# Performance work log

Hardware: AMD Instinct MI355X
Metric: run time of the kernel (lower is better)

## Reference

```python
import jax, jax.numpy as jnp
import numpy as np

N_NODES = 100000
N_EDGES = 1600000
N_GRAPHS = 1024
NODE_F = 100
HID = 64
GLOB_F = 3


def setup_inputs() -> dict:
    key = jax.random.key(0)
    ks = jax.random.split(key, 16)
    s = 0.05
    return {
        "x": jax.random.normal(ks[0], (N_NODES, NODE_F), dtype=jnp.float32),
        "edge_index": jax.random.randint(ks[1], (2, N_EDGES), 0, N_NODES, dtype=jnp.int32),
        "batch": jnp.sort(jax.random.randint(ks[2], (N_NODES,), 0, N_GRAPHS, dtype=jnp.int32)),
        "global_features": jax.random.normal(ks[3], (N_GRAPHS, GLOB_F), dtype=jnp.float32),
        "W1": jax.random.normal(ks[4], (NODE_F, HID), dtype=jnp.float32) * s,
        "b1": jnp.zeros((HID,), dtype=jnp.float32),
        "W2": jax.random.normal(ks[5], (HID, HID), dtype=jnp.float32) * s,
        "b2": jnp.zeros((HID,), dtype=jnp.float32),
        "gW1": jax.random.normal(ks[6], (GLOB_F, HID), dtype=jnp.float32) * s,
        "gb1": jnp.zeros((HID,), dtype=jnp.float32),
        "gW2": jax.random.normal(ks[7], (HID, HID), dtype=jnp.float32) * s,
        "gb2": jnp.zeros((HID,), dtype=jnp.float32),
        "cW1": jax.random.normal(ks[8], (2 * HID, HID), dtype=jnp.float32) * s,
        "cb1": jnp.zeros((HID,), dtype=jnp.float32),
        "cW2": jax.random.normal(ks[9], (HID, 1), dtype=jnp.float32) * s,
        "cb2": jnp.zeros((1,), dtype=jnp.float32),
    }


def gcn_conv(x, src, dst, W, b):
    # PyG GCNConv: add self-loops, symmetric degree normalization, linear transform.
    n = x.shape[0]
    loop = jnp.arange(n, dtype=src.dtype)
    src_sl = jnp.concatenate([src, loop])
    dst_sl = jnp.concatenate([dst, loop])
    deg = jax.ops.segment_sum(jnp.ones_like(dst_sl, dtype=x.dtype), dst_sl, num_segments=n)
    dinv = deg ** -0.5  # deg >= 1 due to self-loops
    norm = dinv[src_sl] * dinv[dst_sl]  # [E+N]
    h = x @ W  # [N, HID]
    msg = h[src_sl] * norm[:, None]
    out = jax.ops.segment_sum(msg, dst_sl, num_segments=n)
    return out + b


def reference(x, edge_index, batch, global_features,
              W1, b1, W2, b2, gW1, gb1, gW2, gb2, cW1, cb1, cW2, cb2):
    src, dst = edge_index[0], edge_index[1]
    h = jax.nn.relu(gcn_conv(x, src, dst, W1, b1))
    # dropout p=0.2 is identity in eval mode
    h = gcn_conv(h, src, dst, W2, b2)
    # global mean pool over graph ids
    sums = jax.ops.segment_sum(h, batch, num_segments=N_GRAPHS)
    cnts = jax.ops.segment_sum(jnp.ones((h.shape[0],), h.dtype), batch, num_segments=N_GRAPHS)
    pooled = sums / jnp.maximum(cnts, 1.0)[:, None]  # [G, HID]
    g = jax.nn.relu(global_features @ gW1 + gb1) @ gW2 + gb2  # [G, HID]
    combined = jnp.concatenate([pooled, g], axis=1)  # [G, 2*HID]
    out = jax.nn.relu(combined @ cW1 + cb1) @ cW2 + cb2  # [G, 1]
    return out
```

## Files before the change

### kernel.cpp

```cpp
#include <hip/hip_runtime.h>

#define N_NODES  100000
#define N_EDGES  1600000
#define N_GRAPHS 1024
#define NODE_F   100
#define HID      64
#define GLOB_F   3

#define CAP      64

#define P_PART     8
#define W_PART     1024
#define R_PART     ((N_NODES + P_PART - 1) / P_PART)
#define CHUNK_PART ((N_EDGES + W_PART - 1) / W_PART)

typedef _Float16 half_t;
typedef __attribute__((ext_vector_type(8))) _Float16 half8;

__global__ void k_bucket(const int* __restrict__ src, const int* __restrict__ dst,
                         int* __restrict__ cnt, int* __restrict__ csrc_pad, int E) {
    int p = blockIdx.x % P_PART;
    int w = blockIdx.x / P_PART;
    int lo_node = p * R_PART;
    int start = w * CHUNK_PART;
    int end = start + CHUNK_PART; if (end > E) end = E;
    for (int i = start + (int)threadIdx.x; i < end; i += 256) {
        int d = dst[i];
        if ((unsigned)(d - lo_node) < (unsigned)R_PART) {
            int pos = atomicAdd(&cnt[d], 1);
            if (pos < CAP) csrc_pad[((size_t)d << 6) + pos] = src[i];
        }
    }
}

template <int K>
__launch_bounds__(256, 3)
__global__ void k_mm(const float* __restrict__ X, const float* __restrict__ W,
                     const int* __restrict__ cnt, half_t* __restrict__ Y, int N) {
    __shared__ float Xs[16 * K];
    __shared__ float dsh[16];
    int tid = threadIdx.x;
    int row0 = blockIdx.x * 16;

    const float4* Xg = reinterpret_cast<const float4*>(X + (size_t)row0 * K);
    float4* Xls = reinterpret_cast<float4*>(Xs);
    for (int i = tid; i < 16 * K / 4; i += 256) Xls[i] = Xg[i];
    if (tid < 16) dsh[tid] = 1.0f / sqrtf((float)(1 + cnt[row0 + tid]));

    int lane = tid & 63;
    int wv = tid >> 6;

    float Wr[K];
#pragma unroll
    for (int k = 0; k < K; ++k) Wr[k] = W[k * HID + lane];
    __syncthreads();

#pragma unroll
    for (int rr = 0; rr < 4; ++rr) {
        int r = row0 + wv * 4 + rr;
        const float4* xrow = reinterpret_cast<const float4*>(&Xs[(wv * 4 + rr) * K]);
        float acc0 = 0.f, acc1 = 0.f, acc2 = 0.f, acc3 = 0.f;
#pragma unroll
        for (int k4 = 0; k4 < K / 4; ++k4) {
            float4 xv = xrow[k4];
            acc0 += xv.x * Wr[k4 * 4 + 0];
            acc1 += xv.y * Wr[k4 * 4 + 1];
            acc2 += xv.z * Wr[k4 * 4 + 2];
            acc3 += xv.w * Wr[k4 * 4 + 3];
        }
        float acc = (acc0 + acc1) + (acc2 + acc3);
        Y[(size_t)r * HID + lane] = (half_t)(acc * dsh[wv * 4 + rr]);
    }
}

template <int RELU>
__global__ void k_gather(const half_t* __restrict__ Hs, const int* __restrict__ cnt,
                         const int* __restrict__ csrc_pad,
                         const float* __restrict__ b, float* __restrict__ outbuf, int N) {
    int tid = threadIdx.x;
    int d = blockIdx.x * 4 + (tid >> 6);
    if (d >= N) return;
    int lane = tid & 63;
    int g = lane >> 3;
    int l = lane & 7;
    int deg = cnt[d];
    int n = deg < CAP ? deg : CAP;
    const int* row = csrc_pad + ((size_t)d << 6);

    float acc[8] = {0, 0, 0, 0, 0, 0, 0, 0};

    int e = 0;
    for (; e + 16 <= n; e += 16) {
        int s0 = row[e + g];
        int s1 = row[e + 8 + g];
        half8 h0 = *reinterpret_cast<const half8*>(Hs + (size_t)s0 * HID + l * 8);
        half8 h1 = *reinterpret_cast<const half8*>(Hs + (size_t)s1 * HID + l * 8);
#pragma unroll
        for (int j = 0; j < 8; ++j) acc[j] += (float)h0[j];
#pragma unroll
        for (int j = 0; j < 8; ++j) acc[j] += (float)h1[j];
    }
    for (; e < n; e += 8) {
        int ee = e + g;
        if (ee < n) {
            int s = row[ee];
            half8 hv = *reinterpret_cast<const half8*>(Hs + (size_t)s * HID + l * 8);
#pragma unroll
            for (int j = 0; j < 8; ++j) acc[j] += (float)hv[j];
        }
    }
    if (g == 0) {
        half8 hv = *reinterpret_cast<const half8*>(Hs + (size_t)d * HID + l * 8);
#pragma unroll
        for (int j = 0; j < 8; ++j) acc[j] += (float)hv[j];
    }
#pragma unroll
    for (int off = 8; off <= 32; off <<= 1) {
#pragma unroll
        for (int j = 0; j < 8; ++j) acc[j] += __shfl_xor(acc[j], off);
    }

    if (g == 0) {
        float dd = 1.0f / sqrtf((float)(1 + deg));
        float v[8];
#pragma unroll
        for (int j = 0; j < 8; ++j) {
            v[j] = acc[j] * dd + b[l * 8 + j];
            if (RELU) v[j] = fmaxf(v[j], 0.0f);
        }
        float4* o = reinterpret_cast<float4*>(outbuf + (size_t)d * HID + l * 8);
        o[0] = make_float4(v[0], v[1], v[2], v[3]);
        o[1] = make_float4(v[4], v[5], v[6], v[7]);
    }
}

__global__ void k_pool(const float* __restrict__ H, const int* __restrict__ batch,
                       float* __restrict__ pooled, int N) {
    int g = blockIdx.x;
    __shared__ int sh_lo, sh_hi;
    __shared__ float red[4][HID];
    if (threadIdx.x == 0) {
        int lo = 0, hi = N;
        while (lo < hi) { int m = (lo + hi) >> 1; if (batch[m] < g) lo = m + 1; else hi = m; }
        sh_lo = lo;
        int lo2 = lo, hi2 = N;
        while (lo2 < hi2) { int m = (lo2 + hi2) >> 1; if (batch[m] < g + 1) lo2 = m + 1; else hi2 = m; }
        sh_hi = lo2;
    }
    __syncthreads();
    int lo = sh_lo, hi = sh_hi;
    int wave = threadIdx.x >> 6, lane = threadIdx.x & 63;
    float acc = 0.0f;
    for (int i = lo + wave; i < hi; i += 4)
        acc += H[(size_t)i * HID + lane];
    red[wave][lane] = acc;
    __syncthreads();
    if (wave == 0) {
        float s = red[0][lane] + red[1][lane] + red[2][lane] + red[3][lane];
        int c = hi - lo;
        pooled[g * HID + lane] = s / (float)(c > 0 ? c : 1);
    }
}

__global__ void k_head(const float* __restrict__ pooled,
                       const float* __restrict__ gf,
                       const float* __restrict__ gW1, const float* __restrict__ gb1,
                       const float* __restrict__ gW2, const float* __restrict__ gb2,
                       const float* __restrict__ cW1, const float* __restrict__ cb1,
                       const float* __restrict__ cW2, const float* __restrict__ cb2,
                       float* __restrict__ out) {
    int g = blockIdx.x;
    int f = threadIdx.x;
    __shared__ float gh[HID];
    __shared__ float comb[2 * HID];

    float a = gb1[f];
#pragma unroll
    for (int k = 0; k < GLOB_F; ++k) a += gf[g * GLOB_F + k] * gW1[k * HID + f];
    gh[f] = fmaxf(a, 0.0f);
    __syncthreads();

    float a2 = gb2[f];
#pragma unroll 8
    for (int k = 0; k < HID; ++k) a2 += gh[k] * gW2[k * HID + f];

    comb[f] = pooled[g * HID + f];
    comb[HID + f] = a2;
    __syncthreads();

    float a3 = cb1[f];
#pragma unroll 8
    for (int k = 0; k < 2 * HID; ++k) a3 += comb[k] * cW1[k * HID + f];
    a3 = fmaxf(a3, 0.0f);

    float prod = a3 * cW2[f];
#pragma unroll
    for (int off = 32; off > 0; off >>= 1) prod += __shfl_down(prod, off);
    if (f == 0) out[g] = prod + cb2[0];
}

extern "C" void kernel_launch(void* const* d_in, const int* in_sizes, int n_in,
                              void* d_out, int out_size, void* d_ws, size_t ws_size,
                              hipStream_t stream) {
    const float* x     = (const float*)d_in[0];
    const int*   ei    = (const int*)d_in[1];
    const int*   batch = (const int*)d_in[2];
    const float* gf    = (const float*)d_in[3];
    const float* W1    = (const float*)d_in[4];
    const float* b1    = (const float*)d_in[5];
    const float* W2    = (const float*)d_in[6];
    const float* b2    = (const float*)d_in[7];
    const float* gW1   = (const float*)d_in[8];
    const float* gb1   = (const float*)d_in[9];
    const float* gW2   = (const float*)d_in[10];
    const float* gb2   = (const float*)d_in[11];
    const float* cW1   = (const float*)d_in[12];
    const float* cb1   = (const float*)d_in[13];
    const float* cW2   = (const float*)d_in[14];
    const float* cb2   = (const float*)d_in[15];
    float* out = (float*)d_out;

    const int* src = ei;
    const int* dst = ei + N_EDGES;

    char* w = (char*)d_ws;
    half_t* Hs       = (half_t*)w; w += (size_t)N_NODES * HID * sizeof(half_t);
    float*  bufB     = (float*)w;  w += (size_t)N_NODES * HID * sizeof(float);
    int*    cnt      = (int*)w;    w += (size_t)N_NODES * sizeof(int);
    int*    csrc_pad = (int*)w;    w += (size_t)N_NODES * CAP * sizeof(int);
    float*  pooled   = (float*)w;  w += (size_t)N_GRAPHS * HID * sizeof(float);

    const int BT = 256;

    hipMemsetAsync(cnt, 0, (size_t)N_NODES * sizeof(int), stream);
    k_bucket<<<P_PART * W_PART, BT, 0, stream>>>(src, dst, cnt, csrc_pad, N_EDGES);

    k_mm<NODE_F><<<N_NODES / 16, BT, 0, stream>>>(x, W1, cnt, Hs, N_NODES);
    k_gather<1><<<(N_NODES + 3) / 4, BT, 0, stream>>>(Hs, cnt, csrc_pad, b1, bufB, N_NODES);

    k_mm<HID><<<N_NODES / 16, BT, 0, stream>>>(bufB, W2, cnt, Hs, N_NODES);
    k_gather<0><<<(N_NODES + 3) / 4, BT, 0, stream>>>(Hs, cnt, csrc_pad, b2, bufB, N_NODES);

    k_pool<<<N_GRAPHS, BT, 0, stream>>>(bufB, batch, pooled, N_NODES);

    k_head<<<N_GRAPHS, HID, 0, stream>>>(pooled, gf, gW1, gb1, gW2, gb2,
                                         cW1, cb1, cW2, cb2, out);
}
```

Baseline: 262.7 us.

## Fuse edge bucketing with first matmul and merge pooling with head

The edge bucketing kernel and the first dense transform now share one launch, with blocks split by index, so the matmul no longer waits on the degree counts. The source-side degree normalization therefore moves into the first gather, which now reads cnt[s] per neighbor to scale each message. Pooling and the MLP head are merged into one kernel, which removes a launch and the pooled intermediate buffer. The cost is an extra random cnt load and rsqrt per edge in the first gather.

```diff
diff --git a/kernel.cpp b/kernel.cpp
--- a/kernel.cpp
+++ b/kernel.cpp
@@ -11,24 +11,64 @@
 
 #define P_PART     8
 #define W_PART     1024
+#define NB_BUCKET  (P_PART * W_PART)
+#define NB_MM      (N_NODES / 16)
 #define R_PART     ((N_NODES + P_PART - 1) / P_PART)
 #define CHUNK_PART ((N_EDGES + W_PART - 1) / W_PART)
 
 typedef _Float16 half_t;
 typedef __attribute__((ext_vector_type(8))) _Float16 half8;
 
-__global__ void k_bucket(const int* __restrict__ src, const int* __restrict__ dst,
-                         int* __restrict__ cnt, int* __restrict__ csrc_pad, int E) {
-    int p = blockIdx.x % P_PART;
-    int w = blockIdx.x / P_PART;
-    int lo_node = p * R_PART;
-    int start = w * CHUNK_PART;
-    int end = start + CHUNK_PART; if (end > E) end = E;
-    for (int i = start + (int)threadIdx.x; i < end; i += 256) {
-        int d = dst[i];
-        if ((unsigned)(d - lo_node) < (unsigned)R_PART) {
-            int pos = atomicAdd(&cnt[d], 1);
-            if (pos < CAP) csrc_pad[((size_t)d << 6) + pos] = src[i];
+__global__ __launch_bounds__(256, 3)
+void k_bucket_mm(const int* __restrict__ src, const int* __restrict__ dst,
+                 int* __restrict__ cnt, int* __restrict__ csrc_pad,
+                 const float* __restrict__ X, const float* __restrict__ W,
+                 half_t* __restrict__ Y, int E) {
+    if (blockIdx.x < NB_BUCKET) {
+        int p = blockIdx.x % P_PART;
+        int w = blockIdx.x / P_PART;
+        int lo_node = p * R_PART;
+        int start = w * CHUNK_PART;
+        int end = start + CHUNK_PART; if (end > E) end = E;
+        for (int i = start + (int)threadIdx.x; i < end; i += 256) {
+            int d = dst[i];
+            if ((unsigned)(d - lo_node) < (unsigned)R_PART) {
+                int pos = atomicAdd(&cnt[d], 1);
+                if (pos < CAP) csrc_pad[((size_t)d << 6) + pos] = src[i];
+            }
+        }
+    } else {
+        __shared__ float Xs[16 * NODE_F];
+        int tid = threadIdx.x;
+        int row0 = (blockIdx.x - NB_BUCKET) * 16;
+
+        const float4* Xg = reinterpret_cast<const float4*>(X + (size_t)row0 * NODE_F);
+        float4* Xls = reinterpret_cast<float4*>(Xs);
+        for (int i = tid; i < 16 * NODE_F / 4; i += 256) Xls[i] = Xg[i];
+
+        int lane = tid & 63;
+        int wv = tid >> 6;
+
+        float Wr[NODE_F];
+#pragma unroll
+        for (int k = 0; k < NODE_F; ++k) Wr[k] = W[k * HID + lane];
+        __syncthreads();
+
+#pragma unroll
+        for (int rr = 0; rr < 4; ++rr) {
+            int r = row0 + wv * 4 + rr;
+            const float4* xrow = reinterpret_cast<const float4*>(&Xs[(wv * 4 + rr) * NODE_F]);
+            float acc0 = 0.f, acc1 = 0.f, acc2 = 0.f, acc3 = 0.f;
+#pragma unroll
+            for (int k4 = 0; k4 < NODE_F / 4; ++k4) {
+                float4 xv = xrow[k4];
+                acc0 += xv.x * Wr[k4 * 4 + 0];
+                acc1 += xv.y * Wr[k4 * 4 + 1];
+                acc2 += xv.z * Wr[k4 * 4 + 2];
+                acc3 += xv.w * Wr[k4 * 4 + 3];
+            }
+            float acc = (acc0 + acc1) + (acc2 + acc3);
+            Y[(size_t)r * HID + lane] = (half_t)acc;
         }
     }
 }
@@ -73,7 +113,7 @@
     }
 }
 
-template <int RELU>
+template <int RELU, int SRCSCALE>
 __global__ void k_gather(const half_t* __restrict__ Hs, const int* __restrict__ cnt,
                          const int* __restrict__ csrc_pad,
                          const float* __restrict__ b, float* __restrict__ outbuf, int N) {
@@ -93,26 +133,33 @@
     for (; e + 16 <= n; e += 16) {
         int s0 = row[e + g];
         int s1 = row[e + 8 + g];
+        float w0 = 1.0f, w1 = 1.0f;
+        if (SRCSCALE) {
+            w0 = 1.0f / sqrtf((float)(1 + cnt[s0]));
+            w1 = 1.0f / sqrtf((float)(1 + cnt[s1]));
+        }
         half8 h0 = *reinterpret_cast<const half8*>(Hs + (size_t)s0 * HID + l * 8);
         half8 h1 = *reinterpret_cast<const half8*>(Hs + (size_t)s1 * HID + l * 8);
 #pragma unroll
-        for (int j = 0; j < 8; ++j) acc[j] += (float)h0[j];
-#pragma unroll
-        for (int j = 0; j < 8; ++j) acc[j] += (float)h1[j];
+        for (int j = 0; j < 8; ++j) acc[j] += w0 * (float)h0[j];
+#pragma unroll
+        for (int j = 0; j < 8; ++j) acc[j] += w1 * (float)h1[j];
     }
     for (; e < n; e += 8) {
         int ee = e + g;
         if (ee < n) {
             int s = row[ee];
+            float ws = SRCSCALE ? (1.0f / sqrtf((float)(1 + cnt[s]))) : 1.0f;
             half8 hv = *reinterpret_cast<const half8*>(Hs + (size_t)s * HID + l * 8);
 #pragma unroll
-            for (int j = 0; j < 8; ++j) acc[j] += (float)hv[j];
+            for (int j = 0; j < 8; ++j) acc[j] += ws * (float)hv[j];
         }
     }
     if (g == 0) {
+        float wd = SRCSCALE ? (1.0f / sqrtf((float)(1 + deg))) : 1.0f;
         half8 hv = *reinterpret_cast<const half8*>(Hs + (size_t)d * HID + l * 8);
 #pragma unroll
-        for (int j = 0; j < 8; ++j) acc[j] += (float)hv[j];
+        for (int j = 0; j < 8; ++j) acc[j] += wd * (float)hv[j];
     }
 #pragma unroll
     for (int off = 8; off <= 32; off <<= 1) {
@@ -134,11 +181,17 @@
     }
 }
 
-__global__ void k_pool(const float* __restrict__ H, const int* __restrict__ batch,
-                       float* __restrict__ pooled, int N) {
+__global__ void k_poolhead(const float* __restrict__ H, const int* __restrict__ batch,
+                           const float* __restrict__ gf,
+                           const float* __restrict__ gW1, const float* __restrict__ gb1,
+                           const float* __restrict__ gW2, const float* __restrict__ gb2,
+                           const float* __restrict__ cW1, const float* __restrict__ cb1,
+                           const float* __restrict__ cW2, const float* __restrict__ cb2,
+                           float* __restrict__ out, int N) {
     int g = blockIdx.x;
     __shared__ int sh_lo, sh_hi;
     __shared__ float red[4][HID];
+    __shared__ float comb[2 * HID];
     if (threadIdx.x == 0) {
         int lo = 0, hi = N;
         while (lo < hi) { int m = (lo + hi) >> 1; if (batch[m] < g) lo = m + 1; else hi = m; }
@@ -155,48 +208,31 @@
         acc += H[(size_t)i * HID + lane];
     red[wave][lane] = acc;
     __syncthreads();
+
     if (wave == 0) {
         float s = red[0][lane] + red[1][lane] + red[2][lane] + red[3][lane];
         int c = hi - lo;
-        pooled[g * HID + lane] = s / (float)(c > 0 ? c : 1);
-    }
-}
-
-__global__ void k_head(const float* __restrict__ pooled,
-                       const float* __restrict__ gf,
-                       const float* __restrict__ gW1, const float* __restrict__ gb1,
-                       const float* __restrict__ gW2, const float* __restrict__ gb2,
-                       const float* __restrict__ cW1, const float* __restrict__ cb1,
-                       const float* __restrict__ cW2, const float* __restrict__ cb2,
-                       float* __restrict__ out) {
-    int g = blockIdx.x;
-    int f = threadIdx.x;
-    __shared__ float gh[HID];
-    __shared__ float comb[2 * HID];
-
-    float a = gb1[f];
-#pragma unroll
-    for (int k = 0; k < GLOB_F; ++k) a += gf[g * GLOB_F + k] * gW1[k * HID + f];
-    gh[f] = fmaxf(a, 0.0f);
-    __syncthreads();
-
-    float a2 = gb2[f];
+        comb[lane] = s / (float)(c > 0 ? c : 1);
+
+        float a = gb1[lane];
+#pragma unroll
+        for (int k = 0; k < GLOB_F; ++k) a += gf[g * GLOB_F + k] * gW1[k * HID + lane];
+        float gh = fmaxf(a, 0.0f);
+        float a2 = gb2[lane];
 #pragma unroll 8
-    for (int k = 0; k < HID; ++k) a2 += gh[k] * gW2[k * HID + f];
-
-    comb[f] = pooled[g * HID + f];
-    comb[HID + f] = a2;
-    __syncthreads();
-
-    float a3 = cb1[f];
+        for (int k = 0; k < HID; ++k) a2 += __shfl(gh, k) * gW2[k * HID + lane];
+        comb[HID + lane] = a2;
+
+        float a3 = cb1[lane];
 #pragma unroll 8
-    for (int k = 0; k < 2 * HID; ++k) a3 += comb[k] * cW1[k * HID + f];
-    a3 = fmaxf(a3, 0.0f);
-
-    float prod = a3 * cW2[f];
-#pragma unroll
-    for (int off = 32; off > 0; off >>= 1) prod += __shfl_down(prod, off);
-    if (f == 0) out[g] = prod + cb2[0];
+        for (int k = 0; k < 2 * HID; ++k) a3 += comb[k] * cW1[k * HID + lane];
+        a3 = fmaxf(a3, 0.0f);
+
+        float prod = a3 * cW2[lane];
+#pragma unroll
+        for (int off = 32; off > 0; off >>= 1) prod += __shfl_down(prod, off);
+        if (lane == 0) out[g] = prod + cb2[0];
+    }
 }
 
 extern "C" void kernel_launch(void* const* d_in, const int* in_sizes, int n_in,
@@ -228,21 +264,18 @@
     float*  bufB     = (float*)w;  w += (size_t)N_NODES * HID * sizeof(float);
     int*    cnt      = (int*)w;    w += (size_t)N_NODES * sizeof(int);
     int*    csrc_pad = (int*)w;    w += (size_t)N_NODES * CAP * sizeof(int);
-    float*  pooled   = (float*)w;  w += (size_t)N_GRAPHS * HID * sizeof(float);
 
     const int BT = 256;
 
     hipMemsetAsync(cnt, 0, (size_t)N_NODES * sizeof(int), stream);
-    k_bucket<<<P_PART * W_PART, BT, 0, stream>>>(src, dst, cnt, csrc_pad, N_EDGES);
-
-    k_mm<NODE_F><<<N_NODES / 16, BT, 0, stream>>>(x, W1, cnt, Hs, N_NODES);
-    k_gather<1><<<(N_NODES + 3) / 4, BT, 0, stream>>>(Hs, cnt, csrc_pad, b1, bufB, N_NODES);
+    k_bucket_mm<<<NB_BUCKET + NB_MM, BT, 0, stream>>>(src, dst, cnt, csrc_pad,
+                                                      x, W1, Hs, N_EDGES);
+
+    k_gather<1, 1><<<(N_NODES + 3) / 4, BT, 0, stream>>>(Hs, cnt, csrc_pad, b1, bufB, N_NODES);
 
     k_mm<HID><<<N_NODES / 16, BT, 0, stream>>>(bufB, W2, cnt, Hs, N_NODES);
-    k_gather<0><<<(N_NODES + 3) / 4, BT, 0, stream>>>(Hs, cnt, csrc_pad, b2, bufB, N_NODES);
-
-    k_pool<<<N_GRAPHS, BT, 0, stream>>>(bufB, batch, pooled, N_NODES);
-
-    k_head<<<N_GRAPHS, HID, 0, stream>>>(pooled, gf, gW1, gb1, gW2, gb2,
-                                         cW1, cb1, cW2, cb2, out);
-}
+    k_gather<0, 0><<<(N_NODES + 3) / 4, BT, 0, stream>>>(Hs, cnt, csrc_pad, b2, bufB, N_NODES);
+
+    k_poolhead<<<N_GRAPHS, BT, 0, stream>>>(bufB, batch, gf, gW1, gb1, gW2, gb2,
+                                            cW1, cb1, cW2, cb2, out, N_NODES);
+}
```

After: 255.9 us. 2.6% less time.
